# Kernel tuning notes

Hardware: AMD Instinct MI355X
Metric: run time of the kernel (lower is better)

Reference implementation:

```python
import jax, jax.numpy as jnp
import numpy as np

STEPS, K, NEW_PTS, GDIM, HDIM = 10, 64, 1152, 256, 128


def setup_inputs() -> dict:
    key = jax.random.key(0)
    ks = jax.random.split(key, 24)
    def w(k, shape):
        return jax.random.normal(k, shape, dtype=jnp.float32) * 0.02
    inp = {
        'points': jax.random.normal(ks[0], (4, 4096, 3), dtype=jnp.float32),
        'gt': jax.random.normal(ks[1], (4, 4096, 3), dtype=jnp.float32),
        # PointNet encoder: 3->64->128->256 (stored [in,out])
        'enc_w1': w(ks[2], (3, 64)),   'enc_b1': jnp.zeros((64,), jnp.float32),
        'enc_w2': w(ks[3], (64, 128)), 'enc_b2': jnp.zeros((128,), jnp.float32),
        'enc_w3': w(ks[4], (128, GDIM)), 'enc_b3': jnp.zeros((GDIM,), jnp.float32),
        # Attention MLP: (3+256+128)->128->1
        'att_w1': w(ks[5], (3 + GDIM + HDIM, 128)), 'att_b1': jnp.zeros((128,), jnp.float32),
        'att_w2': w(ks[6], (128, 1)), 'att_b2': jnp.zeros((1,), jnp.float32),
        # LSTMCell: input 256+3+3=262, hidden 128, gates i,f,g,o
        'lstm_wih': w(ks[7], (GDIM + 6, 4 * HDIM)), 'lstm_whh': w(ks[8], (HDIM, 4 * HDIM)),
        'lstm_bih': jnp.zeros((4 * HDIM,), jnp.float32), 'lstm_bhh': jnp.zeros((4 * HDIM,), jnp.float32),
        # Refiner: 128->128->new_points*3
        'ref_w1': w(ks[9], (HDIM, 128)), 'ref_b1': jnp.zeros((128,), jnp.float32),
        'ref_w2': w(ks[10], (128, NEW_PTS * 3)), 'ref_b2': jnp.zeros((NEW_PTS * 3,), jnp.float32),
    }
    return inp


def _chamfer_sq(x, y):
    # x: [B,N,3], y: [B,M,3]; squared-L2 chamfer, batch-mean (pytorch3d norm=2)
    d2 = (jnp.sum(x * x, -1)[:, :, None] + jnp.sum(y * y, -1)[:, None, :]
          - 2.0 * jnp.einsum('bnd,bmd->bnm', x, y))  # [B,N,M]
    cd = jnp.mean(jnp.min(d2, axis=2), axis=1) + jnp.mean(jnp.min(d2, axis=1), axis=1)
    return jnp.mean(cd)


def _forward(points, gt, enc_w1, enc_b1, enc_w2, enc_b2, enc_w3, enc_b3,
             att_w1, att_b1, att_w2, att_b2,
             lstm_wih, lstm_whh, lstm_bih, lstm_bhh,
             ref_w1, ref_b1, ref_w2, ref_b2):
    B, N0, _ = points.shape
    h = jnp.zeros((B, HDIM), points.dtype)
    c = jnp.zeros((B, HDIM), points.dtype)
    canvas = points
    for _ in range(STEPS):
        # PointNet encoder + max-pool -> global feature [B,GDIM]
        f = jax.nn.relu(canvas @ enc_w1 + enc_b1)
        f = jax.nn.relu(f @ enc_w2 + enc_b2)
        f = f @ enc_w3 + enc_b3
        gfeat = jnp.max(f, axis=1)
        # attention-weighted centroid
        N = canvas.shape[1]
        ctx = jnp.concatenate([
            canvas,
            jnp.broadcast_to(gfeat[:, None, :], (B, N, GDIM)),
            jnp.broadcast_to(h[:, None, :], (B, N, HDIM)),
        ], axis=-1)
        scores = (jax.nn.relu(ctx @ att_w1 + att_b1) @ att_w2 + att_b2)[..., 0]  # [B,N]
        alpha = jax.nn.softmax(scores, axis=1)
        center = jnp.einsum('bn,bnd->bd', alpha, canvas)
        # brute-force KNN around center + gather
        dist = jnp.linalg.norm(canvas - center[:, None, :], axis=-1)  # [B,N]
        _, idx = jax.lax.top_k(-dist, K)  # smallest K
        patch = jnp.take_along_axis(canvas, idx[:, :, None], axis=1)  # [B,K,3]
        patch_feat = jnp.mean(patch - center[:, None, :], axis=1)  # [B,3]
        # LSTM cell (gate order i,f,g,o)
        lstm_in = jnp.concatenate([gfeat, center, patch_feat], axis=1)
        gates = lstm_in @ lstm_wih + lstm_bih + h @ lstm_whh + lstm_bhh
        gi, gf, gg, go = jnp.split(gates, 4, axis=1)
        c = jax.nn.sigmoid(gf) * c + jax.nn.sigmoid(gi) * jnp.tanh(gg)
        h = jax.nn.sigmoid(go) * jnp.tanh(c)
        # refine: generate new patch points around center
        new_pts = (jax.nn.relu(h @ ref_w1 + ref_b1) @ ref_w2 + ref_b2)
        new_pts = new_pts.reshape(B, NEW_PTS, 3) * 0.02 + center[:, None, :]
        canvas = jnp.concatenate([canvas, new_pts], axis=1)
    p_input = canvas[:, :N0, :]
    p_new = canvas[:, N0:, :]
    total_loss = 0.1 * _chamfer_sq(p_input, gt) + 1.0 * _chamfer_sq(p_new, gt)
    return total_loss


def reference(points, gt, enc_w1, enc_b1, enc_w2, enc_b2, enc_w3, enc_b3,
              att_w1, att_b1, att_w2, att_b2,
              lstm_wih, lstm_whh, lstm_bih, lstm_bhh,
              ref_w1, ref_b1, ref_w2, ref_b2):
    return _forward(points, gt, enc_w1, enc_b1, enc_w2, enc_b2, enc_w3, enc_b3,
                    att_w1, att_b1, att_w2, att_b2,
                    lstm_wih, lstm_whh, lstm_bih, lstm_bhh,
                    ref_w1, ref_b1, ref_w2, ref_b2)
```

## Files before the change

kernel.cpp:

```cpp
#include <hip/hip_runtime.h>
#include <math.h>

#define BB 4
#define N0 4096
#define NEWP 1152
#define GD 256
#define HD 128
#define KSEL 64
#define NSTEPS 10
#define NMAX (N0 + NSTEPS*NEWP)
#define NNEW (NSTEPS*NEWP)
#define F2S (BB*N0)

#define OFF_CANVAS 0
#define OFF_MINAB  (OFF_CANVAS + BB*NMAX*3)
#define OFF_MINCD  (OFF_MINAB + 2*BB*N0)
#define OFF_GMAX   (OFF_MINCD + BB*NNEW + BB*N0)
#define OFF_H      (OFF_GMAX + BB*GD)
#define OFF_C      (OFF_H + 2*BB*HD)
#define OFF_ACC    (OFF_C + 2*BB*HD)
#define OFF_CENTER (OFF_ACC + 16)
#define OFF_PART   (OFF_CENTER + 32)
#define OFF_GPART  (OFF_PART + BB*32*8)
#define OFF_F2     (OFF_GPART + 32*BB*512)
#define WS_FLOATS  (OFF_F2 + 128*F2S)

__device__ __forceinline__ unsigned enc_f(float f){
  unsigned u = __float_as_uint(f);
  return (u & 0x80000000u) ? ~u : (u | 0x80000000u);
}
__device__ __forceinline__ float dec_f(unsigned e){
  unsigned u = (e & 0x80000000u) ? (e & 0x7fffffffu) : ~e;
  return __uint_as_float(u);
}
__device__ __forceinline__ float sigm(float x){ return 1.f/(1.f+expf(-x)); }

__device__ __forceinline__ float block_sum(float v, volatile float* red){
#pragma unroll
  for (int s=32;s>0;s>>=1) v += __shfl_down(v, s, 64);
  int lane = threadIdx.x & 63, w = threadIdx.x >> 6, nw = blockDim.x >> 6;
  __syncthreads();
  if (lane==0) red[w] = v;
  __syncthreads();
  if (w==0){
    float x = (lane < nw) ? red[lane] : 0.f;
#pragma unroll
    for (int s=8;s>0;s>>=1) x += __shfl_down(x, s, 64);
    if (lane==0) red[0] = x;
  }
  __syncthreads();
  float r = red[0];
  __syncthreads();
  return r;
}
__device__ __forceinline__ float block_max(float v, volatile float* red){
#pragma unroll
  for (int s=32;s>0;s>>=1) v = fmaxf(v, __shfl_down(v, s, 64));
  int lane = threadIdx.x & 63, w = threadIdx.x >> 6, nw = blockDim.x >> 6;
  __syncthreads();
  if (lane==0) red[w] = v;
  __syncthreads();
  if (w==0){
    float x = (lane < nw) ? red[lane] : -3.4e38f;
#pragma unroll
    for (int s=8;s>0;s>>=1) x = fmaxf(x, __shfl_down(x, s, 64));
    if (lane==0) red[0] = x;
  }
  __syncthreads();
  float r = red[0];
  __syncthreads();
  return r;
}

__global__ __launch_bounds__(512) void init_kernel(
    const float* __restrict__ points,
    float* __restrict__ canvas, unsigned* __restrict__ minAB,
    unsigned* __restrict__ minCD, unsigned* __restrict__ gmax,
    float* __restrict__ h, float* __restrict__ c)
{
  int gid = blockIdx.x*512 + threadIdx.x;
  if (gid < BB*N0*3){
    int b = gid/(N0*3), r = gid - b*(N0*3);
    canvas[(size_t)b*NMAX*3 + r] = points[gid];
  }
  if (gid < 2*BB*N0) minAB[gid] = 0xFFFFFFFFu;
  if (gid < BB*NNEW + BB*N0) minCD[gid] = 0xFFFFFFFFu;
  if (gid < BB*GD) gmax[gid] = 0u;
  if (gid < 2*BB*HD){ h[gid]=0.f; c[gid]=0.f; }
}

__global__ __launch_bounds__(256) void enc12_kernel(
    const float* __restrict__ canvas, const float* __restrict__ w1,
    const float* __restrict__ b1, const float* __restrict__ w2,
    const float* __restrict__ b2, float* __restrict__ f2buf,
    int off, int M)
{
  int b = blockIdx.y;
  int jc = blockIdx.z;
  int i = blockIdx.x*256 + threadIdx.x;
  int ii = (i < M) ? i : 0;
  const float* p = canvas + (size_t)(b*NMAX + off + ii)*3;
  float p0 = p[0], p1 = p[1], p2 = p[2];
  float f1[64];
#pragma unroll
  for (int j=0;j<64;j++)
    f1[j] = fmaxf(0.f, b1[j] + p0*w1[j] + p1*w1[64+j] + p2*w1[128+j]);
  float a[16];
  const float* b2p = b2 + jc*16;
#pragma unroll
  for (int j=0;j<16;j++) a[j] = b2p[j];
#pragma unroll
  for (int k=0;k<64;k++){
    const float* wr = w2 + k*128 + jc*16;
#pragma unroll
    for (int j=0;j<16;j++) a[j] = fmaf(f1[k], wr[j], a[j]);
  }
  if (i < M){
    int base = b*N0 + i;
#pragma unroll
    for (int j=0;j<16;j++)
      f2buf[(size_t)(jc*16 + j)*F2S + base] = fmaxf(a[j], 0.f);
  }
}

__global__ __launch_bounds__(256) void enc3_kernel(
    const float* __restrict__ f2buf, const float* __restrict__ w3,
    const float* __restrict__ b3, unsigned* __restrict__ gmax, int M)
{
  int b = blockIdx.y;
  int dc = blockIdx.z;
  int i = blockIdx.x*256 + threadIdx.x;
  bool act = i < M;
  int ii = act ? i : 0;
  const float* fp = f2buf + b*N0 + ii;
  float a[16];
  const float* b3p = b3 + dc*16;
#pragma unroll
  for (int d=0;d<16;d++) a[d] = b3p[d];
  for (int k=0;k<128;k++){
    float fk = fp[(size_t)k*F2S];
    const float* wr = w3 + k*256 + dc*16;
#pragma unroll
    for (int d=0;d<16;d++) a[d] = fmaf(fk, wr[d], a[d]);
  }
#pragma unroll
  for (int d=0;d<16;d++){
    float v = act ? a[d] : -3.4e38f;
#pragma unroll
    for (int s=32;s>0;s>>=1) v = fmaxf(v, __shfl_down(v, s, 64));
    if ((threadIdx.x & 63) == 0) atomicMax(&gmax[b*GD + dc*16 + d], enc_f(v));
  }
}

__global__ __launch_bounds__(512) void sl_kernel(
    const float* __restrict__ canvas, const float* __restrict__ aw1,
    const float* __restrict__ ab1, const float* __restrict__ aw2,
    const float* __restrict__ ab2, const unsigned* __restrict__ gmax,
    const float* __restrict__ h_in,
    const float* __restrict__ wih, const float* __restrict__ whh,
    float* __restrict__ part, float* __restrict__ gpart, int N, int nch)
{
  __shared__ float sBatt[128];
  __shared__ float red[16];
  __shared__ float sV[BB][12];
  int blk = blockIdx.x;
  int tid = threadIdx.x;
  if (blk < 4*nch){
    int b = blk / nch, ch = blk - b*nch;
    if (tid < 128){
      float a = ab1[tid];
      for (int k=0;k<GD;k++) a += dec_f(gmax[b*GD+k]) * aw1[(3+k)*128 + tid];
      for (int k=0;k<HD;k++) a += h_in[b*HD+k] * aw1[(3+GD+k)*128 + tid];
      sBatt[tid] = a;
    }
    __syncthreads();
    int i = ch*512 + tid;
    bool act = i < N;
    float p0=0.f,p1=0.f,p2=0.f,s=-3.4e38f;
    if (act){
      const float* pp = canvas + (size_t)(b*NMAX + i)*3;
      p0=pp[0]; p1=pp[1]; p2=pp[2];
      s = ab2[0];
      for (int j=0;j<128;j++){
        float v = sBatt[j] + p0*aw1[j] + p1*aw1[128+j] + p2*aw1[256+j];
        s += fmaxf(v, 0.f)*aw2[j];
      }
    }
    float mb = block_max(s, red);
    float e = act ? expf(s - mb) : 0.f;
    float se = block_sum(e, red);
    float wx = block_sum(e*p0, red);
    float wy = block_sum(e*p1, red);
    float wz = block_sum(e*p2, red);
    if (tid==0){
      float* pr = part + (size_t)(b*32 + ch)*8;
      pr[0]=mb; pr[1]=se; pr[2]=wx; pr[3]=wy; pr[4]=wz;
    }
  } else {
    int cc = blk - 4*nch;
    if (tid < BB*12){
      int b = tid/12, j = tid - b*12;
      int r = cc*12 + j;
      sV[b][j] = (r < 256) ? dec_f(gmax[b*GD + r]) : h_in[b*HD + (r-256)];
    }
    __syncthreads();
    float a0=0.f,a1=0.f,a2=0.f,a3=0.f;
#pragma unroll
    for (int j=0;j<12;j++){
      int r = cc*12 + j;
      const float* wr = (r < 256) ? (wih + (size_t)r*512) : (whh + (size_t)(r-256)*512);
      float wvv = wr[tid];
      a0 += sV[0][j]*wvv; a1 += sV[1][j]*wvv;
      a2 += sV[2][j]*wvv; a3 += sV[3][j]*wvv;
    }
    float* gp = gpart + (size_t)cc*(BB*512);
    gp[0*512+tid]=a0; gp[1*512+tid]=a1; gp[2*512+tid]=a2; gp[3*512+tid]=a3;
  }
}

template<int Q>
__global__ __launch_bounds__(1024) void stepA_kernel(
    const float* __restrict__ canvas, const float* __restrict__ part,
    float* __restrict__ centerpf, int N, int nch)
{
  __shared__ float red[16];
  __shared__ float sC[3];
  __shared__ unsigned cbufA[2][16];
  __shared__ unsigned cbufB[2][16];
  __shared__ int tieCnt;
  __shared__ int tieIdx[256];

  int b = blockIdx.x;
  int tid = threadIdx.x;
  int lane = tid & 63, wid = tid >> 6;
  const float* cv = canvas + (size_t)b*NMAX*3;

  float pm=-3.4e38f, pse=0.f, pwx=0.f, pwy=0.f, pwz=0.f;
  if (tid < nch){
    const float* pp = part + (size_t)(b*32 + tid)*8;
    pm=pp[0]; pse=pp[1]; pwx=pp[2]; pwy=pp[3]; pwz=pp[4];
  }
  float M = block_max(pm, red);
  float w = (tid < nch) ? expf(pm - M) : 0.f;
  float se = block_sum(pse*w, red);
  float wx = block_sum(pwx*w, red);
  float wy = block_sum(pwy*w, red);
  float wz = block_sum(pwz*w, red);
  if (tid==0){ sC[0]=wx/se; sC[1]=wy/se; sC[2]=wz/se; }
  __syncthreads();
  float cx=sC[0], cy=sC[1], cz=sC[2];
  if (tid<3) centerpf[b*3+tid] = sC[tid];

  unsigned ur[Q];
#pragma unroll
  for (int q=0;q<Q;q++){
    ur[q] = 0xFFFFFFFFu;
    int i = tid + q*1024;
    if (i < N){
      const float* p = cv + (size_t)i*3;
      float dx=p[0]-cx, dy=p[1]-cy, dz=p[2]-cz;
      ur[q] = __float_as_uint(dx*dx + dy*dy + dz*dz);
    }
  }

  unsigned T = 0u;
  int cntBelow = 0;
  int par = 0;
  {
    unsigned cand = 1u<<30;
    unsigned tc = 0;
#pragma unroll
    for (int q=0;q<Q;q++) tc += (ur[q] < cand) ? 1u : 0u;
#pragma unroll
    for (int s=32;s>0;s>>=1) tc += __shfl_down(tc, s, 64);
    if (lane==0) cbufA[par][wid] = tc;
    __syncthreads();
    unsigned tot = 0;
#pragma unroll
    for (int i2=0;i2<16;i2++) tot += cbufA[par][i2];
    if ((int)tot < KSEL){ T = cand; cntBelow = (int)tot; }
    par ^= 1;
  }
  for (int bit=29; bit>=1; bit-=2){
    unsigned q1 = 1u<<(bit-1);
    unsigned c1 = T + q1, c2 = T + 2u*q1, c3 = T + 3u*q1;
    unsigned ta = 0, tb = 0;
#pragma unroll
    for (int q=0;q<Q;q++){
      unsigned u = ur[q];
      ta += (u < c1 ? 1u : 0u) | (u < c2 ? 0x10000u : 0u);
      tb += (u < c3 ? 1u : 0u);
    }
#pragma unroll
    for (int s=32;s>0;s>>=1){ ta += __shfl_down(ta, s, 64); tb += __shfl_down(tb, s, 64); }
    if (lane==0){ cbufA[par][wid] = ta; cbufB[par][wid] = tb; }
    __syncthreads();
    unsigned sa = 0, sb = 0;
#pragma unroll
    for (int i2=0;i2<16;i2++){ sa += cbufA[par][i2]; sb += cbufB[par][i2]; }
    int n1 = (int)(sa & 0xFFFFu), n2 = (int)(sa >> 16), n3 = (int)sb;
    if (n3 < KSEL){ T = c3; cntBelow = n3; }
    else if (n2 < KSEL){ T = c2; cntBelow = n2; }
    else if (n1 < KSEL){ T = c1; cntBelow = n1; }
    par ^= 1;
  }
  int kneed = KSEL - cntBelow;

  if (tid==0) tieCnt = 0;
  __syncthreads();
  float sx=0.f, sy=0.f, sz=0.f;
#pragma unroll
  for (int q=0;q<Q;q++){
    unsigned u = ur[q];
    if (u < T){
      const float* p = cv + (size_t)(tid + q*1024)*3;
      sx += p[0]; sy += p[1]; sz += p[2];
    } else if (u == T){
      int pos = atomicAdd(&tieCnt, 1);
      if (pos < 256) tieIdx[pos] = tid + q*1024;
    }
  }
  __syncthreads();
  sx = block_sum(sx, red);
  sy = block_sum(sy, red);
  sz = block_sum(sz, red);
  if (tid==0){
    int mm = tieCnt < 256 ? tieCnt : 256;
    for (int t=0;t<kneed;t++){
      int best=-1, bi=0x7fffffff;
      for (int q=0;q<mm;q++){ int v = tieIdx[q]; if (v < bi){ bi=v; best=q; } }
      if (best >= 0){
        tieIdx[best] = 0x7fffffff;
        const float* p = cv + (size_t)bi*3;
        sx += p[0]; sy += p[1]; sz += p[2];
      }
    }
    centerpf[16 + b*3 + 0] = sx/KSEL - cx;
    centerpf[16 + b*3 + 1] = sy/KSEL - cy;
    centerpf[16 + b*3 + 2] = sz/KSEL - cz;
  }
}

__global__ __launch_bounds__(256) void refenc12_kernel(
    float* __restrict__ canvas, const float* __restrict__ gpart,
    const float* __restrict__ centerpf,
    const float* __restrict__ c_in, float* __restrict__ c_out,
    float* __restrict__ h_out,
    const float* __restrict__ wih,
    const float* __restrict__ bih, const float* __restrict__ bhh,
    const float* __restrict__ rw1, const float* __restrict__ rb1,
    const float* __restrict__ rw2, const float* __restrict__ rb2,
    const float* __restrict__ w1, const float* __restrict__ b1,
    const float* __restrict__ w2, const float* __restrict__ b2,
    float* __restrict__ f2buf, int N)
{
  __shared__ float sG[512];
  __shared__ float sH[HD];
  __shared__ float sRf[HD];
  int b = blockIdx.y;
  int jc = blockIdx.z;
  int tid = threadIdx.x;
  float cx = centerpf[b*3+0], cy = centerpf[b*3+1], cz = centerpf[b*3+2];
  float fx = centerpf[16+b*3+0], fy = centerpf[16+b*3+1], fz = centerpf[16+b*3+2];
#pragma unroll
  for (int half=0; half<2; half++){
    int o = tid + half*256;
    float gg = bih[o] + bhh[o];
    for (int cc=0; cc<32; cc++) gg += gpart[(size_t)cc*(BB*512) + b*512 + o];
    gg += cx*wih[(size_t)256*512+o] + cy*wih[(size_t)257*512+o] + cz*wih[(size_t)258*512+o];
    gg += fx*wih[(size_t)259*512+o] + fy*wih[(size_t)260*512+o] + fz*wih[(size_t)261*512+o];
    sG[o] = gg;
  }
  __syncthreads();
  if (tid < HD){
    float gi=sG[tid], gf=sG[128+tid], gg2=sG[256+tid], go=sG[384+tid];
    float cn = sigm(gf)*c_in[b*HD+tid] + sigm(gi)*tanhf(gg2);
    float hn = sigm(go)*tanhf(cn);
    sH[tid] = hn;
    if (blockIdx.x==0 && jc==0){ c_out[b*HD+tid]=cn; h_out[b*HD+tid]=hn; }
  }
  __syncthreads();
  if (tid < HD){
    float a = rb1[tid];
    for (int k=0;k<HD;k++) a += sH[k]*rw1[k*HD + tid];
    sRf[tid] = fmaxf(a, 0.f);
  }
  __syncthreads();
  int i = blockIdx.x*256 + tid;
  bool act = i < NEWP;
  int ic = act ? i : 0;
  float a0 = rb2[3*ic], a1 = rb2[3*ic+1], a2 = rb2[3*ic+2];
  for (int k=0;k<HD;k++){
    const float* wv = rw2 + (size_t)k*(NEWP*3) + 3*ic;
    float hk = sRf[k];
    a0 = fmaf(hk, wv[0], a0); a1 = fmaf(hk, wv[1], a1); a2 = fmaf(hk, wv[2], a2);
  }
  float p0 = fmaf(a0, 0.02f, cx), p1 = fmaf(a1, 0.02f, cy), p2 = fmaf(a2, 0.02f, cz);
  if (act && jc==0){
    float* cp = canvas + ((size_t)b*NMAX + N + i)*3;
    cp[0]=p0; cp[1]=p1; cp[2]=p2;
  }
  float f1[64];
#pragma unroll
  for (int j=0;j<64;j++)
    f1[j] = fmaxf(0.f, b1[j] + p0*w1[j] + p1*w1[64+j] + p2*w1[128+j]);
  float a[16];
  const float* b2p = b2 + jc*16;
#pragma unroll
  for (int j=0;j<16;j++) a[j] = b2p[j];
#pragma unroll
  for (int k=0;k<64;k++){
    const float* wr = w2 + k*128 + jc*16;
#pragma unroll
    for (int j=0;j<16;j++) a[j] = fmaf(f1[k], wr[j], a[j]);
  }
  if (act){
    int base = b*N0 + i;
#pragma unroll
    for (int j=0;j<16;j++)
      f2buf[(size_t)(jc*16 + j)*F2S + base] = fmaxf(a[j], 0.f);
  }
}

__global__ __launch_bounds__(512) void chamfer_kernel(
    const float* __restrict__ canvas, const float* __restrict__ gt,
    unsigned* __restrict__ minAB, unsigned* __restrict__ minCD)
{
  __shared__ float sy0[1024], sy1[1024], sy2[1024], sny[1024];
  int id = blockIdx.x;
  int dir, rem;
  if (id < 32){ dir=0; rem=id; }
  else if (id < 64){ dir=1; rem=id-32; }
  else if (id < 160){ dir=2; rem=id-64; }
  else { dir=3; rem=id-160; }
  int b, xb, yb;
  if (dir < 2){ b = rem>>3; int l = rem&7; xb = l>>2; yb = l&3; }
  else if (dir == 2){ b = rem/24; int l = rem%24; xb = l>>2; yb = l&3; }
  else { b = rem/24; int l = rem%24; xb = l/12; yb = l%12; }

  int Nx, Ny; const float* X; const float* Y; unsigned* mp;
  if (dir==0){      Nx=N0;   Ny=N0;   X=canvas+(size_t)b*NMAX*3;       Y=gt+(size_t)b*N0*3;            mp=minAB + b*N0; }
  else if (dir==1){ Nx=N0;   Ny=N0;   X=gt+(size_t)b*N0*3;             Y=canvas+(size_t)b*NMAX*3;      mp=minAB + BB*N0 + b*N0; }
  else if (dir==2){ Nx=NNEW; Ny=N0;   X=canvas+((size_t)b*NMAX+N0)*3;  Y=gt+(size_t)b*N0*3;            mp=minCD + b*NNEW; }
  else {            Nx=N0;   Ny=NNEW; X=gt+(size_t)b*N0*3;             Y=canvas+((size_t)b*NMAX+N0)*3; mp=minCD + BB*NNEW + b*N0; }

  int xbase = xb*2048;
  int ybase = yb*1024;
  int tn = min(1024, Ny - ybase);
  int tid = threadIdx.x;
  for (int t=tid; t<tn; t+=512){
    const float* yp = Y + (size_t)(ybase+t)*3;
    float y0=yp[0], y1=yp[1], y2=yp[2];
    sy0[t]=-2.f*y0; sy1[t]=-2.f*y1; sy2[t]=-2.f*y2; sny[t]=y0*y0+y1*y1+y2*y2;
  }
  __syncthreads();

  float X0[4],X1[4],X2[4],NXr[4],MN[4]; int XI[4]; bool VA[4];
#pragma unroll
  for (int q=0;q<4;q++){
    int x = xbase + q*512 + tid;
    VA[q] = x < Nx;
    int xc = VA[q] ? x : 0;
    const float* xp = X + (size_t)xc*3;
    X0[q]=xp[0]; X1[q]=xp[1]; X2[q]=xp[2];
    NXr[q] = X0[q]*X0[q] + X1[q]*X1[q] + X2[q]*X2[q];
    MN[q] = 3.4e38f; XI[q] = xc;
  }
  const float4* v0 = (const float4*)sy0;
  const float4* v1 = (const float4*)sy1;
  const float4* v2 = (const float4*)sy2;
  const float4* vn = (const float4*)sny;
  int j4n = tn >> 2;
  for (int j=0;j<j4n;j++){
    float4 a0 = v0[j], a1 = v1[j], a2 = v2[j], an = vn[j];
#pragma unroll
    for (int e=0;e<4;e++){
      float y0 = ((const float*)&a0)[e];
      float y1 = ((const float*)&a1)[e];
      float y2 = ((const float*)&a2)[e];
      float ny = ((const float*)&an)[e];
#pragma unroll
      for (int q=0;q<4;q++){
        float d = fmaf(X0[q], y0, fmaf(X1[q], y1, fmaf(X2[q], y2, ny)));
        MN[q] = fminf(MN[q], d);
      }
    }
  }
  for (int j=j4n*4; j<tn; j++){
    float y0=sy0[j], y1=sy1[j], y2=sy2[j], ny=sny[j];
#pragma unroll
    for (int q=0;q<4;q++){
      float d = fmaf(X0[q], y0, fmaf(X1[q], y1, fmaf(X2[q], y2, ny)));
      MN[q] = fminf(MN[q], d);
    }
  }
#pragma unroll
  for (int q=0;q<4;q++)
    if (VA[q]) atomicMin(&mp[XI[q]], enc_f(MN[q] + NXr[q]));
}

__global__ __launch_bounds__(256) void chamfer_reduce_kernel(
    const unsigned* __restrict__ minAB, const unsigned* __restrict__ minCD,
    float* __restrict__ acc)
{
  __shared__ float red[16];
  int s = blockIdx.x, dir = s>>2, b = s&3;
  const unsigned* mp; int len;
  if (dir==0){      mp=minAB + b*N0;            len=N0; }
  else if (dir==1){ mp=minAB + BB*N0 + b*N0;    len=N0; }
  else if (dir==2){ mp=minCD + b*NNEW;          len=NNEW; }
  else {            mp=minCD + BB*NNEW + b*N0;  len=N0; }
  float v = 0.f;
  for (int i=threadIdx.x;i<len;i+=256) v += dec_f(mp[i]);
  v = block_sum(v, red);
  if (threadIdx.x==0) acc[s] = v;
}

__global__ void finish_kernel(const float* __restrict__ acc, float* __restrict__ out)
{
  if (threadIdx.x == 0 && blockIdx.x == 0){
    float cd1 = 0.f, cd2 = 0.f;
    for (int b=0;b<BB;b++) cd1 += acc[b]/(float)N0 + acc[4+b]/(float)N0;
    for (int b=0;b<BB;b++) cd2 += acc[8+b]/(float)NNEW + acc[12+b]/(float)N0;
    out[0] = 0.1f*(cd1/BB) + 1.0f*(cd2/BB);
  }
}

extern "C" void kernel_launch(void* const* d_in, const int* in_sizes, int n_in,
                              void* d_out, int out_size, void* d_ws, size_t ws_size,
                              hipStream_t stream) {
  (void)in_sizes; (void)n_in; (void)out_size; (void)ws_size;
  const float* points   = (const float*)d_in[0];
  const float* gt       = (const float*)d_in[1];
  const float* enc_w1   = (const float*)d_in[2];
  const float* enc_b1   = (const float*)d_in[3];
  const float* enc_w2   = (const float*)d_in[4];
  const float* enc_b2   = (const float*)d_in[5];
  const float* enc_w3   = (const float*)d_in[6];
  const float* enc_b3   = (const float*)d_in[7];
  const float* att_w1   = (const float*)d_in[8];
  const float* att_b1   = (const float*)d_in[9];
  const float* att_w2   = (const float*)d_in[10];
  const float* att_b2   = (const float*)d_in[11];
  const float* lstm_wih = (const float*)d_in[12];
  const float* lstm_whh = (const float*)d_in[13];
  const float* lstm_bih = (const float*)d_in[14];
  const float* lstm_bhh = (const float*)d_in[15];
  const float* ref_w1   = (const float*)d_in[16];
  const float* ref_b1   = (const float*)d_in[17];
  const float* ref_w2   = (const float*)d_in[18];
  const float* ref_b2   = (const float*)d_in[19];
  float* out = (float*)d_out;

  float* ws       = (float*)d_ws;
  float* canvas   = ws + OFF_CANVAS;
  unsigned* minAB = (unsigned*)(ws + OFF_MINAB);
  unsigned* minCD = (unsigned*)(ws + OFF_MINCD);
  unsigned* gmaxp = (unsigned*)(ws + OFF_GMAX);
  float* hb       = ws + OFF_H;
  float* cb       = ws + OFF_C;
  float* acc      = ws + OFF_ACC;
  float* centerb  = ws + OFF_CENTER;
  float* partb    = ws + OFF_PART;
  float* gpartb   = ws + OFF_GPART;
  float* f2buf    = ws + OFF_F2;

  init_kernel<<<dim3(128), 512, 0, stream>>>(points, canvas, minAB, minCD, gmaxp, hb, cb);
  enc12_kernel<<<dim3(16, BB, 8), 256, 0, stream>>>(canvas, enc_w1, enc_b1, enc_w2, enc_b2, f2buf, 0, N0);
  enc3_kernel<<<dim3(16, BB, 16), 256, 0, stream>>>(f2buf, enc_w3, enc_b3, gmaxp, N0);

  for (int t=0; t<NSTEPS; t++){
    int N   = N0 + t*NEWP;
    int nch = (N + 511) >> 9;
    float* h_in  = hb + (t&1)*BB*HD;
    float* h_out = hb + ((t+1)&1)*BB*HD;
    float* c_in  = cb + (t&1)*BB*HD;
    float* c_out = cb + ((t+1)&1)*BB*HD;
    sl_kernel<<<dim3(4*nch + 32), 512, 0, stream>>>(canvas, att_w1, att_b1, att_w2, att_b2,
                                                    gmaxp, h_in, lstm_wih, lstm_whh,
                                                    partb, gpartb, N, nch);
    if      (N <= 4096)  stepA_kernel<4> <<<dim3(BB), 1024, 0, stream>>>(canvas, partb, centerb, N, nch);
    else if (N <= 8192)  stepA_kernel<8> <<<dim3(BB), 1024, 0, stream>>>(canvas, partb, centerb, N, nch);
    else if (N <= 12288) stepA_kernel<12><<<dim3(BB), 1024, 0, stream>>>(canvas, partb, centerb, N, nch);
    else                 stepA_kernel<16><<<dim3(BB), 1024, 0, stream>>>(canvas, partb, centerb, N, nch);
    refenc12_kernel<<<dim3(5, BB, 8), 256, 0, stream>>>(canvas, gpartb, centerb,
                                                        c_in, c_out, h_out,
                                                        lstm_wih, lstm_bih, lstm_bhh,
                                                        ref_w1, ref_b1, ref_w2, ref_b2,
                                                        enc_w1, enc_b1, enc_w2, enc_b2,
                                                        f2buf, N);
    if (t < NSTEPS-1){
      enc3_kernel<<<dim3(5, BB, 16), 256, 0, stream>>>(f2buf, enc_w3, enc_b3, gmaxp, NEWP);
    }
  }

  chamfer_kernel<<<dim3(256), 512, 0, stream>>>(canvas, gt, minAB, minCD);
  chamfer_reduce_kernel<<<dim3(16), 256, 0, stream>>>(minAB, minCD, acc);
  finish_kernel<<<1, 64, 0, stream>>>(acc, out);
}
```

Baseline: 1.068 ms.

## Fuse all stages into one persistent kernel with a software grid barrier

Replaces the roughly 45 separate kernel launches (init, encoder, per-step attention/LSTM/selection/refine, chamfer, reduce, finish) with a single persistent kernel of 256 blocks. Stages are separated by an atomic-counter grid barrier, and shared memory is reused through a union. The goal is to remove per-launch overhead and the idle gaps between the many small dependent kernels. In exchange, work is forced onto a fixed block count, and correctness relies on all 256 blocks being co-resident. Each barrier also costs global atomics and spinning.

```diff
diff --git a/kernel.cpp b/kernel.cpp
--- a/kernel.cpp
+++ b/kernel.cpp
@@ -11,6 +11,9 @@
 #define NMAX (N0 + NSTEPS*NEWP)
 #define NNEW (NSTEPS*NEWP)
 #define F2S (BB*N0)
+
+#define NBLK 256
+#define NTHR 512
 
 #define OFF_CANVAS 0
 #define OFF_MINAB  (OFF_CANVAS + BB*NMAX*3)
@@ -72,453 +75,486 @@
   return r;
 }
 
-__global__ __launch_bounds__(512) void init_kernel(
-    const float* __restrict__ points,
-    float* __restrict__ canvas, unsigned* __restrict__ minAB,
-    unsigned* __restrict__ minCD, unsigned* __restrict__ gmax,
-    float* __restrict__ h, float* __restrict__ c)
-{
-  int gid = blockIdx.x*512 + threadIdx.x;
-  if (gid < BB*N0*3){
-    int b = gid/(N0*3), r = gid - b*(N0*3);
-    canvas[(size_t)b*NMAX*3 + r] = points[gid];
-  }
-  if (gid < 2*BB*N0) minAB[gid] = 0xFFFFFFFFu;
-  if (gid < BB*NNEW + BB*N0) minCD[gid] = 0xFFFFFFFFu;
-  if (gid < BB*GD) gmax[gid] = 0u;
-  if (gid < 2*BB*HD){ h[gid]=0.f; c[gid]=0.f; }
-}
-
-__global__ __launch_bounds__(256) void enc12_kernel(
-    const float* __restrict__ canvas, const float* __restrict__ w1,
-    const float* __restrict__ b1, const float* __restrict__ w2,
-    const float* __restrict__ b2, float* __restrict__ f2buf,
-    int off, int M)
-{
-  int b = blockIdx.y;
-  int jc = blockIdx.z;
-  int i = blockIdx.x*256 + threadIdx.x;
-  int ii = (i < M) ? i : 0;
-  const float* p = canvas + (size_t)(b*NMAX + off + ii)*3;
-  float p0 = p[0], p1 = p[1], p2 = p[2];
-  float f1[64];
-#pragma unroll
-  for (int j=0;j<64;j++)
-    f1[j] = fmaxf(0.f, b1[j] + p0*w1[j] + p1*w1[64+j] + p2*w1[128+j]);
-  float a[16];
-  const float* b2p = b2 + jc*16;
-#pragma unroll
-  for (int j=0;j<16;j++) a[j] = b2p[j];
-#pragma unroll
-  for (int k=0;k<64;k++){
-    const float* wr = w2 + k*128 + jc*16;
-#pragma unroll
-    for (int j=0;j<16;j++) a[j] = fmaf(f1[k], wr[j], a[j]);
-  }
-  if (i < M){
-    int base = b*N0 + i;
-#pragma unroll
-    for (int j=0;j<16;j++)
-      f2buf[(size_t)(jc*16 + j)*F2S + base] = fmaxf(a[j], 0.f);
-  }
-}
-
-__global__ __launch_bounds__(256) void enc3_kernel(
-    const float* __restrict__ f2buf, const float* __restrict__ w3,
-    const float* __restrict__ b3, unsigned* __restrict__ gmax, int M)
-{
-  int b = blockIdx.y;
-  int dc = blockIdx.z;
-  int i = blockIdx.x*256 + threadIdx.x;
-  bool act = i < M;
-  int ii = act ? i : 0;
-  const float* fp = f2buf + b*N0 + ii;
-  float a[16];
-  const float* b3p = b3 + dc*16;
-#pragma unroll
-  for (int d=0;d<16;d++) a[d] = b3p[d];
-  for (int k=0;k<128;k++){
-    float fk = fp[(size_t)k*F2S];
-    const float* wr = w3 + k*256 + dc*16;
-#pragma unroll
-    for (int d=0;d<16;d++) a[d] = fmaf(fk, wr[d], a[d]);
-  }
-#pragma unroll
-  for (int d=0;d<16;d++){
-    float v = act ? a[d] : -3.4e38f;
-#pragma unroll
-    for (int s=32;s>0;s>>=1) v = fmaxf(v, __shfl_down(v, s, 64));
-    if ((threadIdx.x & 63) == 0) atomicMax(&gmax[b*GD + dc*16 + d], enc_f(v));
-  }
-}
-
-__global__ __launch_bounds__(512) void sl_kernel(
-    const float* __restrict__ canvas, const float* __restrict__ aw1,
-    const float* __restrict__ ab1, const float* __restrict__ aw2,
-    const float* __restrict__ ab2, const unsigned* __restrict__ gmax,
-    const float* __restrict__ h_in,
+__device__ __align__(128) unsigned g_cnt = 0u;
+__device__ __align__(128) unsigned g_gen = 0u;
+
+__device__ __forceinline__ void gsync(){
+  __syncthreads();
+  if (threadIdx.x == 0){
+    unsigned g  = __hip_atomic_load(&g_gen, __ATOMIC_RELAXED, __HIP_MEMORY_SCOPE_AGENT);
+    unsigned od = __hip_atomic_fetch_add(&g_cnt, 1u, __ATOMIC_ACQ_REL, __HIP_MEMORY_SCOPE_AGENT);
+    if (od == (unsigned)(NBLK-1)){
+      __hip_atomic_store(&g_cnt, 0u, __ATOMIC_RELAXED, __HIP_MEMORY_SCOPE_AGENT);
+      __hip_atomic_fetch_add(&g_gen, 1u, __ATOMIC_ACQ_REL, __HIP_MEMORY_SCOPE_AGENT);
+    } else {
+      while (__hip_atomic_load(&g_gen, __ATOMIC_RELAXED, __HIP_MEMORY_SCOPE_AGENT) == g)
+        __builtin_amdgcn_s_sleep(1);
+    }
+    __threadfence();
+  }
+  __syncthreads();
+}
+
+struct alignas(16) SU {
+  union {
+    struct { float sy0[1024], sy1[1024], sy2[1024], sny[1024]; } ch;
+    struct { float sBatt[128]; float sV[BB][12]; float red[16]; } sl;
+    struct { float red[16]; float sC[3]; unsigned cbufA[2][8]; unsigned cbufB[2][8];
+             int tieCnt; int tieIdx[256]; } sa;
+    struct { float sG[512]; float sH[HD]; float sRf[HD]; } re;
+    struct { float red[16]; } rd;
+  } u;
+};
+
+__global__ __launch_bounds__(NTHR, 2) void mega_kernel(
+    const float* __restrict__ points, const float* __restrict__ gt,
+    const float* __restrict__ w1,  const float* __restrict__ b1,
+    const float* __restrict__ w2,  const float* __restrict__ b2,
+    const float* __restrict__ w3,  const float* __restrict__ b3,
+    const float* __restrict__ aw1, const float* __restrict__ ab1,
+    const float* __restrict__ aw2, const float* __restrict__ ab2,
     const float* __restrict__ wih, const float* __restrict__ whh,
-    float* __restrict__ part, float* __restrict__ gpart, int N, int nch)
-{
-  __shared__ float sBatt[128];
-  __shared__ float red[16];
-  __shared__ float sV[BB][12];
-  int blk = blockIdx.x;
-  int tid = threadIdx.x;
-  if (blk < 4*nch){
-    int b = blk / nch, ch = blk - b*nch;
-    if (tid < 128){
-      float a = ab1[tid];
-      for (int k=0;k<GD;k++) a += dec_f(gmax[b*GD+k]) * aw1[(3+k)*128 + tid];
-      for (int k=0;k<HD;k++) a += h_in[b*HD+k] * aw1[(3+GD+k)*128 + tid];
-      sBatt[tid] = a;
-    }
-    __syncthreads();
-    int i = ch*512 + tid;
-    bool act = i < N;
-    float p0=0.f,p1=0.f,p2=0.f,s=-3.4e38f;
-    if (act){
-      const float* pp = canvas + (size_t)(b*NMAX + i)*3;
-      p0=pp[0]; p1=pp[1]; p2=pp[2];
-      s = ab2[0];
-      for (int j=0;j<128;j++){
-        float v = sBatt[j] + p0*aw1[j] + p1*aw1[128+j] + p2*aw1[256+j];
-        s += fmaxf(v, 0.f)*aw2[j];
-      }
-    }
-    float mb = block_max(s, red);
-    float e = act ? expf(s - mb) : 0.f;
-    float se = block_sum(e, red);
-    float wx = block_sum(e*p0, red);
-    float wy = block_sum(e*p1, red);
-    float wz = block_sum(e*p2, red);
-    if (tid==0){
-      float* pr = part + (size_t)(b*32 + ch)*8;
-      pr[0]=mb; pr[1]=se; pr[2]=wx; pr[3]=wy; pr[4]=wz;
-    }
-  } else {
-    int cc = blk - 4*nch;
-    if (tid < BB*12){
-      int b = tid/12, j = tid - b*12;
-      int r = cc*12 + j;
-      sV[b][j] = (r < 256) ? dec_f(gmax[b*GD + r]) : h_in[b*HD + (r-256)];
-    }
-    __syncthreads();
-    float a0=0.f,a1=0.f,a2=0.f,a3=0.f;
-#pragma unroll
-    for (int j=0;j<12;j++){
-      int r = cc*12 + j;
-      const float* wr = (r < 256) ? (wih + (size_t)r*512) : (whh + (size_t)(r-256)*512);
-      float wvv = wr[tid];
-      a0 += sV[0][j]*wvv; a1 += sV[1][j]*wvv;
-      a2 += sV[2][j]*wvv; a3 += sV[3][j]*wvv;
-    }
-    float* gp = gpart + (size_t)cc*(BB*512);
-    gp[0*512+tid]=a0; gp[1*512+tid]=a1; gp[2*512+tid]=a2; gp[3*512+tid]=a3;
-  }
-}
-
-template<int Q>
-__global__ __launch_bounds__(1024) void stepA_kernel(
-    const float* __restrict__ canvas, const float* __restrict__ part,
-    float* __restrict__ centerpf, int N, int nch)
-{
-  __shared__ float red[16];
-  __shared__ float sC[3];
-  __shared__ unsigned cbufA[2][16];
-  __shared__ unsigned cbufB[2][16];
-  __shared__ int tieCnt;
-  __shared__ int tieIdx[256];
-
-  int b = blockIdx.x;
-  int tid = threadIdx.x;
-  int lane = tid & 63, wid = tid >> 6;
-  const float* cv = canvas + (size_t)b*NMAX*3;
-
-  float pm=-3.4e38f, pse=0.f, pwx=0.f, pwy=0.f, pwz=0.f;
-  if (tid < nch){
-    const float* pp = part + (size_t)(b*32 + tid)*8;
-    pm=pp[0]; pse=pp[1]; pwx=pp[2]; pwy=pp[3]; pwz=pp[4];
-  }
-  float M = block_max(pm, red);
-  float w = (tid < nch) ? expf(pm - M) : 0.f;
-  float se = block_sum(pse*w, red);
-  float wx = block_sum(pwx*w, red);
-  float wy = block_sum(pwy*w, red);
-  float wz = block_sum(pwz*w, red);
-  if (tid==0){ sC[0]=wx/se; sC[1]=wy/se; sC[2]=wz/se; }
-  __syncthreads();
-  float cx=sC[0], cy=sC[1], cz=sC[2];
-  if (tid<3) centerpf[b*3+tid] = sC[tid];
-
-  unsigned ur[Q];
-#pragma unroll
-  for (int q=0;q<Q;q++){
-    ur[q] = 0xFFFFFFFFu;
-    int i = tid + q*1024;
-    if (i < N){
-      const float* p = cv + (size_t)i*3;
-      float dx=p[0]-cx, dy=p[1]-cy, dz=p[2]-cz;
-      ur[q] = __float_as_uint(dx*dx + dy*dy + dz*dz);
-    }
-  }
-
-  unsigned T = 0u;
-  int cntBelow = 0;
-  int par = 0;
-  {
-    unsigned cand = 1u<<30;
-    unsigned tc = 0;
-#pragma unroll
-    for (int q=0;q<Q;q++) tc += (ur[q] < cand) ? 1u : 0u;
-#pragma unroll
-    for (int s=32;s>0;s>>=1) tc += __shfl_down(tc, s, 64);
-    if (lane==0) cbufA[par][wid] = tc;
-    __syncthreads();
-    unsigned tot = 0;
-#pragma unroll
-    for (int i2=0;i2<16;i2++) tot += cbufA[par][i2];
-    if ((int)tot < KSEL){ T = cand; cntBelow = (int)tot; }
-    par ^= 1;
-  }
-  for (int bit=29; bit>=1; bit-=2){
-    unsigned q1 = 1u<<(bit-1);
-    unsigned c1 = T + q1, c2 = T + 2u*q1, c3 = T + 3u*q1;
-    unsigned ta = 0, tb = 0;
-#pragma unroll
-    for (int q=0;q<Q;q++){
-      unsigned u = ur[q];
-      ta += (u < c1 ? 1u : 0u) | (u < c2 ? 0x10000u : 0u);
-      tb += (u < c3 ? 1u : 0u);
-    }
-#pragma unroll
-    for (int s=32;s>0;s>>=1){ ta += __shfl_down(ta, s, 64); tb += __shfl_down(tb, s, 64); }
-    if (lane==0){ cbufA[par][wid] = ta; cbufB[par][wid] = tb; }
-    __syncthreads();
-    unsigned sa = 0, sb = 0;
-#pragma unroll
-    for (int i2=0;i2<16;i2++){ sa += cbufA[par][i2]; sb += cbufB[par][i2]; }
-    int n1 = (int)(sa & 0xFFFFu), n2 = (int)(sa >> 16), n3 = (int)sb;
-    if (n3 < KSEL){ T = c3; cntBelow = n3; }
-    else if (n2 < KSEL){ T = c2; cntBelow = n2; }
-    else if (n1 < KSEL){ T = c1; cntBelow = n1; }
-    par ^= 1;
-  }
-  int kneed = KSEL - cntBelow;
-
-  if (tid==0) tieCnt = 0;
-  __syncthreads();
-  float sx=0.f, sy=0.f, sz=0.f;
-#pragma unroll
-  for (int q=0;q<Q;q++){
-    unsigned u = ur[q];
-    if (u < T){
-      const float* p = cv + (size_t)(tid + q*1024)*3;
-      sx += p[0]; sy += p[1]; sz += p[2];
-    } else if (u == T){
-      int pos = atomicAdd(&tieCnt, 1);
-      if (pos < 256) tieIdx[pos] = tid + q*1024;
-    }
-  }
-  __syncthreads();
-  sx = block_sum(sx, red);
-  sy = block_sum(sy, red);
-  sz = block_sum(sz, red);
-  if (tid==0){
-    int mm = tieCnt < 256 ? tieCnt : 256;
-    for (int t=0;t<kneed;t++){
-      int best=-1, bi=0x7fffffff;
-      for (int q=0;q<mm;q++){ int v = tieIdx[q]; if (v < bi){ bi=v; best=q; } }
-      if (best >= 0){
-        tieIdx[best] = 0x7fffffff;
-        const float* p = cv + (size_t)bi*3;
-        sx += p[0]; sy += p[1]; sz += p[2];
-      }
-    }
-    centerpf[16 + b*3 + 0] = sx/KSEL - cx;
-    centerpf[16 + b*3 + 1] = sy/KSEL - cy;
-    centerpf[16 + b*3 + 2] = sz/KSEL - cz;
-  }
-}
-
-__global__ __launch_bounds__(256) void refenc12_kernel(
-    float* __restrict__ canvas, const float* __restrict__ gpart,
-    const float* __restrict__ centerpf,
-    const float* __restrict__ c_in, float* __restrict__ c_out,
-    float* __restrict__ h_out,
-    const float* __restrict__ wih,
     const float* __restrict__ bih, const float* __restrict__ bhh,
     const float* __restrict__ rw1, const float* __restrict__ rb1,
     const float* __restrict__ rw2, const float* __restrict__ rb2,
-    const float* __restrict__ w1, const float* __restrict__ b1,
-    const float* __restrict__ w2, const float* __restrict__ b2,
-    float* __restrict__ f2buf, int N)
+    float* __restrict__ out, float* __restrict__ ws)
 {
-  __shared__ float sG[512];
-  __shared__ float sH[HD];
-  __shared__ float sRf[HD];
-  int b = blockIdx.y;
-  int jc = blockIdx.z;
-  int tid = threadIdx.x;
-  float cx = centerpf[b*3+0], cy = centerpf[b*3+1], cz = centerpf[b*3+2];
-  float fx = centerpf[16+b*3+0], fy = centerpf[16+b*3+1], fz = centerpf[16+b*3+2];
-#pragma unroll
-  for (int half=0; half<2; half++){
-    int o = tid + half*256;
-    float gg = bih[o] + bhh[o];
-    for (int cc=0; cc<32; cc++) gg += gpart[(size_t)cc*(BB*512) + b*512 + o];
-    gg += cx*wih[(size_t)256*512+o] + cy*wih[(size_t)257*512+o] + cz*wih[(size_t)258*512+o];
-    gg += fx*wih[(size_t)259*512+o] + fy*wih[(size_t)260*512+o] + fz*wih[(size_t)261*512+o];
-    sG[o] = gg;
-  }
-  __syncthreads();
-  if (tid < HD){
-    float gi=sG[tid], gf=sG[128+tid], gg2=sG[256+tid], go=sG[384+tid];
-    float cn = sigm(gf)*c_in[b*HD+tid] + sigm(gi)*tanhf(gg2);
-    float hn = sigm(go)*tanhf(cn);
-    sH[tid] = hn;
-    if (blockIdx.x==0 && jc==0){ c_out[b*HD+tid]=cn; h_out[b*HD+tid]=hn; }
-  }
-  __syncthreads();
-  if (tid < HD){
-    float a = rb1[tid];
-    for (int k=0;k<HD;k++) a += sH[k]*rw1[k*HD + tid];
-    sRf[tid] = fmaxf(a, 0.f);
-  }
-  __syncthreads();
-  int i = blockIdx.x*256 + tid;
-  bool act = i < NEWP;
-  int ic = act ? i : 0;
-  float a0 = rb2[3*ic], a1 = rb2[3*ic+1], a2 = rb2[3*ic+2];
-  for (int k=0;k<HD;k++){
-    const float* wv = rw2 + (size_t)k*(NEWP*3) + 3*ic;
-    float hk = sRf[k];
-    a0 = fmaf(hk, wv[0], a0); a1 = fmaf(hk, wv[1], a1); a2 = fmaf(hk, wv[2], a2);
-  }
-  float p0 = fmaf(a0, 0.02f, cx), p1 = fmaf(a1, 0.02f, cy), p2 = fmaf(a2, 0.02f, cz);
-  if (act && jc==0){
-    float* cp = canvas + ((size_t)b*NMAX + N + i)*3;
-    cp[0]=p0; cp[1]=p1; cp[2]=p2;
-  }
-  float f1[64];
-#pragma unroll
-  for (int j=0;j<64;j++)
-    f1[j] = fmaxf(0.f, b1[j] + p0*w1[j] + p1*w1[64+j] + p2*w1[128+j]);
-  float a[16];
-  const float* b2p = b2 + jc*16;
-#pragma unroll
-  for (int j=0;j<16;j++) a[j] = b2p[j];
-#pragma unroll
-  for (int k=0;k<64;k++){
-    const float* wr = w2 + k*128 + jc*16;
-#pragma unroll
-    for (int j=0;j<16;j++) a[j] = fmaf(f1[k], wr[j], a[j]);
-  }
-  if (act){
+  __shared__ SU su;
+  const int tid = threadIdx.x;
+  const int blk = blockIdx.x;
+
+  float* canvas   = ws + OFF_CANVAS;
+  unsigned* minAB = (unsigned*)(ws + OFF_MINAB);
+  unsigned* minCD = (unsigned*)(ws + OFF_MINCD);
+  unsigned* gmax  = (unsigned*)(ws + OFF_GMAX);
+  float* hb       = ws + OFF_H;
+  float* cb       = ws + OFF_C;
+  float* acc      = ws + OFF_ACC;
+  float* centerb  = ws + OFF_CENTER;
+  float* partb    = ws + OFF_PART;
+  float* gpartb   = ws + OFF_GPART;
+  float* f2buf    = ws + OFF_F2;
+
+  {
+    int gid = blk*NTHR + tid;
+    if (gid < BB*N0*3){
+      int b = gid/(N0*3), r = gid - b*(N0*3);
+      canvas[(size_t)b*NMAX*3 + r] = points[gid];
+    }
+    if (gid < 2*BB*N0) minAB[gid] = 0xFFFFFFFFu;
+    if (gid < BB*NNEW + BB*N0) minCD[gid] = 0xFFFFFFFFu;
+    if (gid < BB*GD) gmax[gid] = 0u;
+    if (gid < 2*BB*HD){ hb[gid]=0.f; cb[gid]=0.f; }
+
+    int pc = blk>>5, b = (blk>>3)&3, jc = blk&7;
+    int i = pc*NTHR + tid;
+    const float* p = points + (size_t)(b*N0 + i)*3;
+    float p0 = p[0], p1 = p[1], p2 = p[2];
+    float f1[64];
+#pragma unroll
+    for (int j=0;j<64;j++)
+      f1[j] = fmaxf(0.f, b1[j] + p0*w1[j] + p1*w1[64+j] + p2*w1[128+j]);
+    float a[16];
+    const float* b2p = b2 + jc*16;
+#pragma unroll
+    for (int j=0;j<16;j++) a[j] = b2p[j];
+#pragma unroll
+    for (int k=0;k<64;k++){
+      const float* wr = w2 + k*128 + jc*16;
+#pragma unroll
+      for (int j=0;j<16;j++) a[j] = fmaf(f1[k], wr[j], a[j]);
+    }
     int base = b*N0 + i;
 #pragma unroll
     for (int j=0;j<16;j++)
       f2buf[(size_t)(jc*16 + j)*F2S + base] = fmaxf(a[j], 0.f);
   }
-}
-
-__global__ __launch_bounds__(512) void chamfer_kernel(
-    const float* __restrict__ canvas, const float* __restrict__ gt,
-    unsigned* __restrict__ minAB, unsigned* __restrict__ minCD)
-{
-  __shared__ float sy0[1024], sy1[1024], sy2[1024], sny[1024];
-  int id = blockIdx.x;
-  int dir, rem;
-  if (id < 32){ dir=0; rem=id; }
-  else if (id < 64){ dir=1; rem=id-32; }
-  else if (id < 160){ dir=2; rem=id-64; }
-  else { dir=3; rem=id-160; }
-  int b, xb, yb;
-  if (dir < 2){ b = rem>>3; int l = rem&7; xb = l>>2; yb = l&3; }
-  else if (dir == 2){ b = rem/24; int l = rem%24; xb = l>>2; yb = l&3; }
-  else { b = rem/24; int l = rem%24; xb = l/12; yb = l%12; }
-
-  int Nx, Ny; const float* X; const float* Y; unsigned* mp;
-  if (dir==0){      Nx=N0;   Ny=N0;   X=canvas+(size_t)b*NMAX*3;       Y=gt+(size_t)b*N0*3;            mp=minAB + b*N0; }
-  else if (dir==1){ Nx=N0;   Ny=N0;   X=gt+(size_t)b*N0*3;             Y=canvas+(size_t)b*NMAX*3;      mp=minAB + BB*N0 + b*N0; }
-  else if (dir==2){ Nx=NNEW; Ny=N0;   X=canvas+((size_t)b*NMAX+N0)*3;  Y=gt+(size_t)b*N0*3;            mp=minCD + b*NNEW; }
-  else {            Nx=N0;   Ny=NNEW; X=gt+(size_t)b*N0*3;             Y=canvas+((size_t)b*NMAX+N0)*3; mp=minCD + BB*NNEW + b*N0; }
-
-  int xbase = xb*2048;
-  int ybase = yb*1024;
-  int tn = min(1024, Ny - ybase);
-  int tid = threadIdx.x;
-  for (int t=tid; t<tn; t+=512){
-    const float* yp = Y + (size_t)(ybase+t)*3;
-    float y0=yp[0], y1=yp[1], y2=yp[2];
-    sy0[t]=-2.f*y0; sy1[t]=-2.f*y1; sy2[t]=-2.f*y2; sny[t]=y0*y0+y1*y1+y2*y2;
-  }
-  __syncthreads();
-
-  float X0[4],X1[4],X2[4],NXr[4],MN[4]; int XI[4]; bool VA[4];
-#pragma unroll
-  for (int q=0;q<4;q++){
-    int x = xbase + q*512 + tid;
-    VA[q] = x < Nx;
-    int xc = VA[q] ? x : 0;
-    const float* xp = X + (size_t)xc*3;
-    X0[q]=xp[0]; X1[q]=xp[1]; X2[q]=xp[2];
-    NXr[q] = X0[q]*X0[q] + X1[q]*X1[q] + X2[q]*X2[q];
-    MN[q] = 3.4e38f; XI[q] = xc;
-  }
-  const float4* v0 = (const float4*)sy0;
-  const float4* v1 = (const float4*)sy1;
-  const float4* v2 = (const float4*)sy2;
-  const float4* vn = (const float4*)sny;
-  int j4n = tn >> 2;
-  for (int j=0;j<j4n;j++){
-    float4 a0 = v0[j], a1 = v1[j], a2 = v2[j], an = vn[j];
-#pragma unroll
-    for (int e=0;e<4;e++){
-      float y0 = ((const float*)&a0)[e];
-      float y1 = ((const float*)&a1)[e];
-      float y2 = ((const float*)&a2)[e];
-      float ny = ((const float*)&an)[e];
+  gsync();
+
+  {
+    int combo = blk & 63, pc = blk >> 6;
+    int b = combo>>4, dc = combo&15;
+#pragma unroll
+    for (int pp=0; pp<2; pp++){
+      int i = pc*1024 + pp*512 + tid;
+      const float* fp = f2buf + b*N0 + i;
+      float a[16];
+      const float* b3p = b3 + dc*16;
+#pragma unroll
+      for (int d=0;d<16;d++) a[d] = b3p[d];
+      for (int k=0;k<128;k++){
+        float fk = fp[(size_t)k*F2S];
+        const float* wr = w3 + k*256 + dc*16;
+#pragma unroll
+        for (int d=0;d<16;d++) a[d] = fmaf(fk, wr[d], a[d]);
+      }
+#pragma unroll
+      for (int d=0;d<16;d++){
+        float v = a[d];
+#pragma unroll
+        for (int s2=32;s2>0;s2>>=1) v = fmaxf(v, __shfl_down(v, s2, 64));
+        if ((tid & 63) == 0) atomicMax(&gmax[b*GD + dc*16 + d], enc_f(v));
+      }
+    }
+  }
+  gsync();
+
+  for (int t=0; t<NSTEPS; t++){
+    int N   = N0 + t*NEWP;
+    int nch = (N + 511) >> 9;
+    float* h_in  = hb + (t&1)*BB*HD;
+    float* h_out = hb + ((t+1)&1)*BB*HD;
+    float* c_in  = cb + (t&1)*BB*HD;
+    float* c_out = cb + ((t+1)&1)*BB*HD;
+
+    if (blk < 4*nch){
+      int b = blk / nch, ch = blk - b*nch;
+      if (tid < 128){
+        float a = ab1[tid];
+        for (int k=0;k<GD;k++) a += dec_f(gmax[b*GD+k]) * aw1[(3+k)*128 + tid];
+        for (int k=0;k<HD;k++) a += h_in[b*HD+k] * aw1[(3+GD+k)*128 + tid];
+        su.u.sl.sBatt[tid] = a;
+      }
+      __syncthreads();
+      int i = ch*512 + tid;
+      bool act = i < N;
+      float p0=0.f,p1=0.f,p2=0.f,s=-3.4e38f;
+      if (act){
+        const float* pp = canvas + (size_t)(b*NMAX + i)*3;
+        p0=pp[0]; p1=pp[1]; p2=pp[2];
+        s = ab2[0];
+        for (int j=0;j<128;j++){
+          float v = su.u.sl.sBatt[j] + p0*aw1[j] + p1*aw1[128+j] + p2*aw1[256+j];
+          s += fmaxf(v, 0.f)*aw2[j];
+        }
+      }
+      float mb = block_max(s, su.u.sl.red);
+      float e = act ? expf(s - mb) : 0.f;
+      float se = block_sum(e, su.u.sl.red);
+      float wx = block_sum(e*p0, su.u.sl.red);
+      float wy = block_sum(e*p1, su.u.sl.red);
+      float wz = block_sum(e*p2, su.u.sl.red);
+      if (tid==0){
+        float* pr = partb + (size_t)(b*32 + ch)*8;
+        pr[0]=mb; pr[1]=se; pr[2]=wx; pr[3]=wy; pr[4]=wz;
+      }
+    }
+    gsync();
+
+    if (blk < 4){
+      int b = blk;
+      const float* cv = canvas + (size_t)b*NMAX*3;
+      int lane = tid & 63, wid = tid >> 6;
+
+      float pm=-3.4e38f, pse=0.f, pwx=0.f, pwy=0.f, pwz=0.f;
+      if (tid < nch){
+        const float* pp = partb + (size_t)(b*32 + tid)*8;
+        pm=pp[0]; pse=pp[1]; pwx=pp[2]; pwy=pp[3]; pwz=pp[4];
+      }
+      float M = block_max(pm, su.u.sa.red);
+      float w = (tid < nch) ? expf(pm - M) : 0.f;
+      float se = block_sum(pse*w, su.u.sa.red);
+      float wx = block_sum(pwx*w, su.u.sa.red);
+      float wy = block_sum(pwy*w, su.u.sa.red);
+      float wz = block_sum(pwz*w, su.u.sa.red);
+      if (tid==0){ su.u.sa.sC[0]=wx/se; su.u.sa.sC[1]=wy/se; su.u.sa.sC[2]=wz/se; }
+      __syncthreads();
+      float cx=su.u.sa.sC[0], cy=su.u.sa.sC[1], cz=su.u.sa.sC[2];
+      if (tid<3) centerb[b*3+tid] = su.u.sa.sC[tid];
+
+      unsigned ur[32];
+#pragma unroll
+      for (int q=0;q<32;q++){
+        ur[q] = 0xFFFFFFFFu;
+        int i = tid + q*NTHR;
+        if (i < N){
+          const float* p = cv + (size_t)i*3;
+          float dx=p[0]-cx, dy=p[1]-cy, dz=p[2]-cz;
+          ur[q] = __float_as_uint(dx*dx + dy*dy + dz*dz);
+        }
+      }
+
+      unsigned T = 0u;
+      int cntBelow = 0;
+      int par = 0;
+      {
+        unsigned cand = 1u<<30;
+        unsigned tc = 0;
+#pragma unroll
+        for (int q=0;q<32;q++) tc += (ur[q] < cand) ? 1u : 0u;
+#pragma unroll
+        for (int s2=32;s2>0;s2>>=1) tc += __shfl_down(tc, s2, 64);
+        if (lane==0) su.u.sa.cbufA[par][wid] = tc;
+        __syncthreads();
+        unsigned tot = 0;
+#pragma unroll
+        for (int i2=0;i2<8;i2++) tot += su.u.sa.cbufA[par][i2];
+        if ((int)tot < KSEL){ T = cand; cntBelow = (int)tot; }
+        par ^= 1;
+      }
+      for (int bit=29; bit>=1; bit-=2){
+        unsigned q1 = 1u<<(bit-1);
+        unsigned c1 = T + q1, c2 = T + 2u*q1, c3 = T + 3u*q1;
+        unsigned ta = 0, tb = 0;
+#pragma unroll
+        for (int q=0;q<32;q++){
+          unsigned u = ur[q];
+          ta += (u < c1 ? 1u : 0u) | (u < c2 ? 0x10000u : 0u);
+          tb += (u < c3 ? 1u : 0u);
+        }
+#pragma unroll
+        for (int s2=32;s2>0;s2>>=1){ ta += __shfl_down(ta, s2, 64); tb += __shfl_down(tb, s2, 64); }
+        if (lane==0){ su.u.sa.cbufA[par][wid] = ta; su.u.sa.cbufB[par][wid] = tb; }
+        __syncthreads();
+        unsigned sa2 = 0, sb2 = 0;
+#pragma unroll
+        for (int i2=0;i2<8;i2++){ sa2 += su.u.sa.cbufA[par][i2]; sb2 += su.u.sa.cbufB[par][i2]; }
+        int n1 = (int)(sa2 & 0xFFFFu), n2 = (int)(sa2 >> 16), n3 = (int)sb2;
+        if (n3 < KSEL){ T = c3; cntBelow = n3; }
+        else if (n2 < KSEL){ T = c2; cntBelow = n2; }
+        else if (n1 < KSEL){ T = c1; cntBelow = n1; }
+        par ^= 1;
+      }
+      int kneed = KSEL - cntBelow;
+
+      if (tid==0) su.u.sa.tieCnt = 0;
+      __syncthreads();
+      float sx=0.f, sy=0.f, sz=0.f;
+#pragma unroll
+      for (int q=0;q<32;q++){
+        unsigned uu = ur[q];
+        if (uu < T){
+          const float* p = cv + (size_t)(tid + q*NTHR)*3;
+          sx += p[0]; sy += p[1]; sz += p[2];
+        } else if (uu == T){
+          int pos = atomicAdd(&su.u.sa.tieCnt, 1);
+          if (pos < 256) su.u.sa.tieIdx[pos] = tid + q*NTHR;
+        }
+      }
+      __syncthreads();
+      sx = block_sum(sx, su.u.sa.red);
+      sy = block_sum(sy, su.u.sa.red);
+      sz = block_sum(sz, su.u.sa.red);
+      if (tid==0){
+        int mm = su.u.sa.tieCnt < 256 ? su.u.sa.tieCnt : 256;
+        for (int tt=0; tt<kneed; tt++){
+          int best=-1, bi=0x7fffffff;
+          for (int q=0;q<mm;q++){ int v = su.u.sa.tieIdx[q]; if (v < bi){ bi=v; best=q; } }
+          if (best >= 0){
+            su.u.sa.tieIdx[best] = 0x7fffffff;
+            const float* p = cv + (size_t)bi*3;
+            sx += p[0]; sy += p[1]; sz += p[2];
+          }
+        }
+        centerb[16 + b*3 + 0] = sx/KSEL - cx;
+        centerb[16 + b*3 + 1] = sy/KSEL - cy;
+        centerb[16 + b*3 + 2] = sz/KSEL - cz;
+      }
+    } else if (blk < 36){
+      int cc = blk - 4;
+      if (tid < BB*12){
+        int b = tid/12, j = tid - b*12;
+        int r = cc*12 + j;
+        su.u.sl.sV[b][j] = (r < 256) ? dec_f(gmax[b*GD + r]) : h_in[b*HD + (r-256)];
+      }
+      __syncthreads();
+      float a0=0.f,a1=0.f,a2=0.f,a3=0.f;
+#pragma unroll
+      for (int j=0;j<12;j++){
+        int r = cc*12 + j;
+        const float* wr = (r < 256) ? (wih + (size_t)r*512) : (whh + (size_t)(r-256)*512);
+        float wvv = wr[tid];
+        a0 += su.u.sl.sV[0][j]*wvv; a1 += su.u.sl.sV[1][j]*wvv;
+        a2 += su.u.sl.sV[2][j]*wvv; a3 += su.u.sl.sV[3][j]*wvv;
+      }
+      float* gp = gpartb + (size_t)cc*(BB*512);
+      gp[0*512+tid]=a0; gp[1*512+tid]=a1; gp[2*512+tid]=a2; gp[3*512+tid]=a3;
+    }
+    gsync();
+
+    if (blk < 96){
+      int bx = blk>>5, b = (blk>>3)&3, jc = blk&7;
+      float cx = centerb[b*3+0], cy = centerb[b*3+1], cz = centerb[b*3+2];
+      float fx = centerb[16+b*3+0], fy = centerb[16+b*3+1], fz = centerb[16+b*3+2];
+      {
+        int o = tid;
+        float gg = bih[o] + bhh[o];
+        for (int cc2=0; cc2<32; cc2++) gg += gpartb[(size_t)cc2*(BB*512) + b*512 + o];
+        gg += cx*wih[(size_t)256*512+o] + cy*wih[(size_t)257*512+o] + cz*wih[(size_t)258*512+o];
+        gg += fx*wih[(size_t)259*512+o] + fy*wih[(size_t)260*512+o] + fz*wih[(size_t)261*512+o];
+        su.u.re.sG[o] = gg;
+      }
+      __syncthreads();
+      if (tid < HD){
+        float gi=su.u.re.sG[tid], gf=su.u.re.sG[128+tid], gg2=su.u.re.sG[256+tid], go=su.u.re.sG[384+tid];
+        float cn = sigm(gf)*c_in[b*HD+tid] + sigm(gi)*tanhf(gg2);
+        float hn = sigm(go)*tanhf(cn);
+        su.u.re.sH[tid] = hn;
+        if (bx==0 && jc==0){ c_out[b*HD+tid]=cn; h_out[b*HD+tid]=hn; }
+      }
+      __syncthreads();
+      if (tid < HD){
+        float a = rb1[tid];
+        for (int k=0;k<HD;k++) a += su.u.re.sH[k]*rw1[k*HD + tid];
+        su.u.re.sRf[tid] = fmaxf(a, 0.f);
+      }
+      __syncthreads();
+      int i = bx*NTHR + tid;
+      bool act = i < NEWP;
+      int ic = act ? i : 0;
+      float a0 = rb2[3*ic], a1 = rb2[3*ic+1], a2 = rb2[3*ic+2];
+      for (int k=0;k<HD;k++){
+        const float* wv = rw2 + (size_t)k*(NEWP*3) + 3*ic;
+        float hk = su.u.re.sRf[k];
+        a0 = fmaf(hk, wv[0], a0); a1 = fmaf(hk, wv[1], a1); a2 = fmaf(hk, wv[2], a2);
+      }
+      float p0 = fmaf(a0, 0.02f, cx), p1 = fmaf(a1, 0.02f, cy), p2 = fmaf(a2, 0.02f, cz);
+      if (act && jc==0){
+        float* cp = canvas + ((size_t)b*NMAX + N + i)*3;
+        cp[0]=p0; cp[1]=p1; cp[2]=p2;
+      }
+      float f1[64];
+#pragma unroll
+      for (int j=0;j<64;j++)
+        f1[j] = fmaxf(0.f, b1[j] + p0*w1[j] + p1*w1[64+j] + p2*w1[128+j]);
+      float a[16];
+      const float* b2p = b2 + jc*16;
+#pragma unroll
+      for (int j=0;j<16;j++) a[j] = b2p[j];
+#pragma unroll
+      for (int k=0;k<64;k++){
+        const float* wr = w2 + k*128 + jc*16;
+#pragma unroll
+        for (int j=0;j<16;j++) a[j] = fmaf(f1[k], wr[j], a[j]);
+      }
+      if (act){
+        int base = b*N0 + i;
+#pragma unroll
+        for (int j=0;j<16;j++)
+          f2buf[(size_t)(jc*16 + j)*F2S + base] = fmaxf(a[j], 0.f);
+      }
+    }
+    gsync();
+
+    if (t < NSTEPS-1){
+      if (blk < 192){
+        int combo = blk & 63, pc = blk >> 6;
+        int b = combo>>4, dc = combo&15;
+        int i = pc*NTHR + tid;
+        bool act = i < NEWP;
+        int ii = act ? i : 0;
+        const float* fp = f2buf + b*N0 + ii;
+        float a[16];
+        const float* b3p = b3 + dc*16;
+#pragma unroll
+        for (int d=0;d<16;d++) a[d] = b3p[d];
+        for (int k=0;k<128;k++){
+          float fk = fp[(size_t)k*F2S];
+          const float* wr = w3 + k*256 + dc*16;
+#pragma unroll
+          for (int d=0;d<16;d++) a[d] = fmaf(fk, wr[d], a[d]);
+        }
+#pragma unroll
+        for (int d=0;d<16;d++){
+          float v = act ? a[d] : -3.4e38f;
+#pragma unroll
+          for (int s2=32;s2>0;s2>>=1) v = fmaxf(v, __shfl_down(v, s2, 64));
+          if ((tid & 63) == 0) atomicMax(&gmax[b*GD + dc*16 + d], enc_f(v));
+        }
+      }
+      gsync();
+    }
+  }
+
+  {
+    int id = blk;
+    int dir, rem;
+    if (id < 32){ dir=0; rem=id; }
+    else if (id < 64){ dir=1; rem=id-32; }
+    else if (id < 160){ dir=2; rem=id-64; }
+    else { dir=3; rem=id-160; }
+    int b, xb, yb;
+    if (dir < 2){ b = rem>>3; int l = rem&7; xb = l>>2; yb = l&3; }
+    else if (dir == 2){ b = rem/24; int l = rem%24; xb = l>>2; yb = l&3; }
+    else { b = rem/24; int l = rem%24; xb = l/12; yb = l%12; }
+
+    int Nx, Ny; const float* X; const float* Y; unsigned* mp;
+    if (dir==0){      Nx=N0;   Ny=N0;   X=canvas+(size_t)b*NMAX*3;       Y=gt+(size_t)b*N0*3;            mp=minAB + b*N0; }
+    else if (dir==1){ Nx=N0;   Ny=N0;   X=gt+(size_t)b*N0*3;             Y=canvas+(size_t)b*NMAX*3;      mp=minAB + BB*N0 + b*N0; }
+    else if (dir==2){ Nx=NNEW; Ny=N0;   X=canvas+((size_t)b*NMAX+N0)*3;  Y=gt+(size_t)b*N0*3;            mp=minCD + b*NNEW; }
+    else {            Nx=N0;   Ny=NNEW; X=gt+(size_t)b*N0*3;             Y=canvas+((size_t)b*NMAX+N0)*3; mp=minCD + BB*NNEW + b*N0; }
+
+    int xbase = xb*2048;
+    int ybase = yb*1024;
+    int tn = min(1024, Ny - ybase);
+    for (int tt=tid; tt<tn; tt+=NTHR){
+      const float* yp = Y + (size_t)(ybase+tt)*3;
+      float y0=yp[0], y1=yp[1], y2=yp[2];
+      su.u.ch.sy0[tt]=-2.f*y0; su.u.ch.sy1[tt]=-2.f*y1; su.u.ch.sy2[tt]=-2.f*y2;
+      su.u.ch.sny[tt]=y0*y0+y1*y1+y2*y2;
+    }
+    __syncthreads();
+
+    float X0[4],X1[4],X2[4],NXr[4],MN[4]; int XI[4]; bool VA[4];
+#pragma unroll
+    for (int q=0;q<4;q++){
+      int x = xbase + q*512 + tid;
+      VA[q] = x < Nx;
+      int xc = VA[q] ? x : 0;
+      const float* xp = X + (size_t)xc*3;
+      X0[q]=xp[0]; X1[q]=xp[1]; X2[q]=xp[2];
+      NXr[q] = X0[q]*X0[q] + X1[q]*X1[q] + X2[q]*X2[q];
+      MN[q] = 3.4e38f; XI[q] = xc;
+    }
+    const float4* v0 = (const float4*)su.u.ch.sy0;
+    const float4* v1 = (const float4*)su.u.ch.sy1;
+    const float4* v2 = (const float4*)su.u.ch.sy2;
+    const float4* vn = (const float4*)su.u.ch.sny;
+    int j4n = tn >> 2;
+    for (int j=0;j<j4n;j++){
+      float4 a0 = v0[j], a1 = v1[j], a2 = v2[j], an = vn[j];
+#pragma unroll
+      for (int e=0;e<4;e++){
+        float y0 = ((const float*)&a0)[e];
+        float y1 = ((const float*)&a1)[e];
+        float y2 = ((const float*)&a2)[e];
+        float ny = ((const float*)&an)[e];
+#pragma unroll
+        for (int q=0;q<4;q++){
+          float d = fmaf(X0[q], y0, fmaf(X1[q], y1, fmaf(X2[q], y2, ny)));
+          MN[q] = fminf(MN[q], d);
+        }
+      }
+    }
+    for (int j=j4n*4; j<tn; j++){
+      float y0=su.u.ch.sy0[j], y1=su.u.ch.sy1[j], y2=su.u.ch.sy2[j], ny=su.u.ch.sny[j];
 #pragma unroll
       for (int q=0;q<4;q++){
         float d = fmaf(X0[q], y0, fmaf(X1[q], y1, fmaf(X2[q], y2, ny)));
         MN[q] = fminf(MN[q], d);
       }
     }
-  }
-  for (int j=j4n*4; j<tn; j++){
-    float y0=sy0[j], y1=sy1[j], y2=sy2[j], ny=sny[j];
-#pragma unroll
-    for (int q=0;q<4;q++){
-      float d = fmaf(X0[q], y0, fmaf(X1[q], y1, fmaf(X2[q], y2, ny)));
-      MN[q] = fminf(MN[q], d);
-    }
-  }
-#pragma unroll
-  for (int q=0;q<4;q++)
-    if (VA[q]) atomicMin(&mp[XI[q]], enc_f(MN[q] + NXr[q]));
-}
-
-__global__ __launch_bounds__(256) void chamfer_reduce_kernel(
-    const unsigned* __restrict__ minAB, const unsigned* __restrict__ minCD,
-    float* __restrict__ acc)
-{
-  __shared__ float red[16];
-  int s = blockIdx.x, dir = s>>2, b = s&3;
-  const unsigned* mp; int len;
-  if (dir==0){      mp=minAB + b*N0;            len=N0; }
-  else if (dir==1){ mp=minAB + BB*N0 + b*N0;    len=N0; }
-  else if (dir==2){ mp=minCD + b*NNEW;          len=NNEW; }
-  else {            mp=minCD + BB*NNEW + b*N0;  len=N0; }
-  float v = 0.f;
-  for (int i=threadIdx.x;i<len;i+=256) v += dec_f(mp[i]);
-  v = block_sum(v, red);
-  if (threadIdx.x==0) acc[s] = v;
-}
-
-__global__ void finish_kernel(const float* __restrict__ acc, float* __restrict__ out)
-{
-  if (threadIdx.x == 0 && blockIdx.x == 0){
+#pragma unroll
+    for (int q=0;q<4;q++)
+      if (VA[q]) atomicMin(&mp[XI[q]], enc_f(MN[q] + NXr[q]));
+  }
+  gsync();
+
+  if (blk < 16){
+    int s = blk, dir = s>>2, b = s&3;
+    const unsigned* mp; int len;
+    if (dir==0){      mp=minAB + b*N0;            len=N0; }
+    else if (dir==1){ mp=minAB + BB*N0 + b*N0;    len=N0; }
+    else if (dir==2){ mp=minCD + b*NNEW;          len=NNEW; }
+    else {            mp=minCD + BB*NNEW + b*N0;  len=N0; }
+    float v = 0.f;
+    for (int i=tid;i<len;i+=NTHR) v += dec_f(mp[i]);
+    v = block_sum(v, su.u.rd.red);
+    if (tid==0) acc[s] = v;
+  }
+  gsync();
+
+  if (blk == 0 && tid == 0){
     float cd1 = 0.f, cd2 = 0.f;
     for (int b=0;b<BB;b++) cd1 += acc[b]/(float)N0 + acc[4+b]/(float)N0;
     for (int b=0;b<BB;b++) cd2 += acc[8+b]/(float)NNEW + acc[12+b]/(float)N0;
@@ -551,50 +587,13 @@
   const float* ref_w2   = (const float*)d_in[18];
   const float* ref_b2   = (const float*)d_in[19];
   float* out = (float*)d_out;
-
-  float* ws       = (float*)d_ws;
-  float* canvas   = ws + OFF_CANVAS;
-  unsigned* minAB = (unsigned*)(ws + OFF_MINAB);
-  unsigned* minCD = (unsigned*)(ws + OFF_MINCD);
-  unsigned* gmaxp = (unsigned*)(ws + OFF_GMAX);
-  float* hb       = ws + OFF_H;
-  float* cb       = ws + OFF_C;
-  float* acc      = ws + OFF_ACC;
-  float* centerb  = ws + OFF_CENTER;
-  float* partb    = ws + OFF_PART;
-  float* gpartb   = ws + OFF_GPART;
-  float* f2buf    = ws + OFF_F2;
-
-  init_kernel<<<dim3(128), 512, 0, stream>>>(points, canvas, minAB, minCD, gmaxp, hb, cb);
-  enc12_kernel<<<dim3(16, BB, 8), 256, 0, stream>>>(canvas, enc_w1, enc_b1, enc_w2, enc_b2, f2buf, 0, N0);
-  enc3_kernel<<<dim3(16, BB, 16), 256, 0, stream>>>(f2buf, enc_w3, enc_b3, gmaxp, N0);
-
-  for (int t=0; t<NSTEPS; t++){
-    int N   = N0 + t*NEWP;
-    int nch = (N + 511) >> 9;
-    float* h_in  = hb + (t&1)*BB*HD;
-    float* h_out = hb + ((t+1)&1)*BB*HD;
-    float* c_in  = cb + (t&1)*BB*HD;
-    float* c_out = cb + ((t+1)&1)*BB*HD;
-    sl_kernel<<<dim3(4*nch + 32), 512, 0, stream>>>(canvas, att_w1, att_b1, att_w2, att_b2,
-                                                    gmaxp, h_in, lstm_wih, lstm_whh,
-                                                    partb, gpartb, N, nch);
-    if      (N <= 4096)  stepA_kernel<4> <<<dim3(BB), 1024, 0, stream>>>(canvas, partb, centerb, N, nch);
-    else if (N <= 8192)  stepA_kernel<8> <<<dim3(BB), 1024, 0, stream>>>(canvas, partb, centerb, N, nch);
-    else if (N <= 12288) stepA_kernel<12><<<dim3(BB), 1024, 0, stream>>>(canvas, partb, centerb, N, nch);
-    else                 stepA_kernel<16><<<dim3(BB), 1024, 0, stream>>>(canvas, partb, centerb, N, nch);
-    refenc12_kernel<<<dim3(5, BB, 8), 256, 0, stream>>>(canvas, gpartb, centerb,
-                                                        c_in, c_out, h_out,
-                                                        lstm_wih, lstm_bih, lstm_bhh,
-                                                        ref_w1, ref_b1, ref_w2, ref_b2,
-                                                        enc_w1, enc_b1, enc_w2, enc_b2,
-                                                        f2buf, N);
-    if (t < NSTEPS-1){
-      enc3_kernel<<<dim3(5, BB, 16), 256, 0, stream>>>(f2buf, enc_w3, enc_b3, gmaxp, NEWP);
-    }
-  }
-
-  chamfer_kernel<<<dim3(256), 512, 0, stream>>>(canvas, gt, minAB, minCD);
-  chamfer_reduce_kernel<<<dim3(16), 256, 0, stream>>>(minAB, minCD, acc);
-  finish_kernel<<<1, 64, 0, stream>>>(acc, out);
-}
+  float* ws  = (float*)d_ws;
+
+  mega_kernel<<<dim3(NBLK), NTHR, 0, stream>>>(
+      points, gt,
+      enc_w1, enc_b1, enc_w2, enc_b2, enc_w3, enc_b3,
+      att_w1, att_b1, att_w2, att_b2,
+      lstm_wih, lstm_whh, lstm_bih, lstm_bhh,
+      ref_w1, ref_b1, ref_w2, ref_b2,
+      out, ws);
+}
```

Measured after the change: 3.200 ms. 3x slower.
